# Performance work log

Hardware: AMD Instinct MI355X
Metric: run time of the kernel (lower is better)

Reference implementation:

```python
import jax, jax.numpy as jnp
import numpy as np
import math

DIM = 4096      # hidden size
NH = 32         # query heads
NKV = 8         # kv heads (GQA)
HD = 128        # head dim
SW = 4096       # sliding window / cache length
B = 8           # batch (decode)
START_POS = 2047
PAD_LEN = min(((START_POS + 1 + 31) // 32) * 32, SW)  # nearest_32 -> 2048
ROPE_THETA = 10000.0


def _rotation_matrix(pos, dhead, theta=ROPE_THETA):
    # freqs_to_rotation_matrix: block-diagonal 2x2 rotations, applied as q @ R
    freqs = 1.0 / (theta ** (np.arange(0, dhead, 2, dtype=np.float64) / dhead))
    ang = pos * freqs
    cos, sin = np.cos(ang), np.sin(ang)
    rot = np.zeros((dhead, dhead), dtype=np.float32)
    ev = np.arange(0, dhead, 2)
    od = ev + 1
    rot[ev, ev] = cos
    rot[od, od] = cos
    rot[ev, od] = -sin
    rot[od, ev] = sin
    return rot


def setup_inputs() -> dict:
    key = jax.random.key(0)
    ks = jax.random.split(key, 8)
    s = 0.02
    x = jax.random.normal(ks[0], (1, 1, B, DIM), jnp.float32)
    wq = jax.random.normal(ks[1], (DIM, NH * HD), jnp.float32) * s
    wk = jax.random.normal(ks[2], (DIM, NKV * HD), jnp.float32) * s
    wv = jax.random.normal(ks[3], (DIM, NKV * HD), jnp.float32) * s
    wo = jax.random.normal(ks[4], (NH * HD, DIM), jnp.float32) * s
    # true RoPE rotation matrix for the current position, same for all batch rows
    rot = jnp.asarray(_rotation_matrix(START_POS, HD))
    rot_mat = jnp.broadcast_to(rot, (1, B, HD, HD))
    # KV cache: valid history in [0, START_POS), rest is garbage that gets masked
    cache_k = jax.random.normal(ks[5], (B, NKV, SW, HD), jnp.float32) * s
    cache_v = jax.random.normal(ks[6], (B, NKV, SW, HD), jnp.float32) * s
    # additive mask: 0 for positions <= start_pos, finfo.min after
    neg = jnp.finfo(jnp.float32).min
    mask_row = jnp.where(jnp.arange(PAD_LEN) <= START_POS, 0.0, neg).astype(jnp.float32)
    attn_mask = jnp.broadcast_to(mask_row, (1, NH, B, PAD_LEN))
    return {
        "x": x, "wq": wq, "wk": wk, "wv": wv, "wo": wo,
        "rot_mat": rot_mat, "cache_k": cache_k, "cache_v": cache_v,
        "attn_mask": attn_mask, "start_pos": START_POS,
    }


def reference(x, wq, wk, wv, wo, rot_mat, cache_k, cache_v, attn_mask, start_pos):
    scale = 1.0 / math.sqrt(HD)
    xb = x[0, 0]                                  # (B, DIM)
    # fused QKV projection
    q = (xb @ wq).reshape(B, NH, HD)              # (B, NH, HD)
    k = (xb @ wk).reshape(B, NKV, HD)             # (B, NKV, HD)
    v = (xb @ wv).reshape(B, NKV, HD)             # (B, NKV, HD)
    # RoPE via explicit rotation-matrix matmul (per batch row)
    rm = rot_mat[0]                               # (B, HD, HD)
    q = jnp.einsum('bhd,bde->bhe', q, rm)
    k = jnp.einsum('bgd,bde->bge', k, rm)
    # update_cache at position `oldest` (= start_pos since start_pos < sliding_window)
    ck = cache_k.at[:, :, start_pos].set(k)
    cv = cache_v.at[:, :, start_pos].set(v)
    keys = ck[:, :, :PAD_LEN]                     # (B, NKV, L, HD)
    vals = cv[:, :, :PAD_LEN]                     # (B, NKV, L, HD)
    # grouped attention: NH query heads share NKV kv heads
    qg = q.reshape(B, NKV, NH // NKV, HD)
    scores = jnp.einsum('bgqd,bgld->bgql', qg, keys) * scale
    # attn_mask: (1, NH, B, L) -> (B, NKV, NH//NKV, L)
    mask = attn_mask[0].transpose(1, 0, 2).reshape(B, NKV, NH // NKV, PAD_LEN)
    probs = jax.nn.softmax(scores + mask, axis=-1)
    out = jnp.einsum('bgql,bgld->bgqd', probs, vals).reshape(B, NH * HD)
    dense = out @ wo                              # (B, DIM)
    return dense.reshape(1, 1, B, DIM)
```

## Files before the change

### kernel.cpp

```cpp
#include <hip/hip_runtime.h>
#include <math.h>

#define DIM 4096
#define NH 32
#define NKV 8
#define HD 128
#define B_ 8
#define SW 4096
#define PAD_LEN 2048
#define GQ 4
#define KSPLIT 16
#define KCHUNK 256
#define QKV_COLS (DIM + 2 * NKV * HD)
#define LCHUNK 256
#define NLCHUNK (PAD_LEN / LCHUNK)
#define SCALE 0.08838834764831845f

#define OFF_QKVP   0
#define OFF_Q      (OFF_QKVP + KSPLIT * B_ * QKV_COLS)
#define OFF_K      (OFF_Q + B_ * DIM)
#define OFF_V      (OFF_K + B_ * NKV * HD)
#define OFF_AP     (OFF_V + B_ * NKV * HD)
#define OFF_AO     (OFF_AP + B_ * NKV * NLCHUNK * GQ * (HD + 2))
#define OFF_OP     (OFF_AO + B_ * DIM)

__global__ void qkv_partial(const float* __restrict__ x,
                            const float* __restrict__ wq,
                            const float* __restrict__ wk,
                            const float* __restrict__ wv,
                            float* __restrict__ part) {
    __shared__ float xs[B_][KCHUNK];
    const int tid = threadIdx.x;
    const int col = blockIdx.x * 256 + tid;
    const int k0  = blockIdx.y * KCHUNK;

    #pragma unroll
    for (int i = 0; i < (B_ * KCHUNK) / 256; ++i) {
        int idx = i * 256 + tid;
        int r   = idx >> 8;
        int kk  = idx & (KCHUNK - 1);
        xs[r][kk] = x[r * DIM + k0 + kk];
    }
    __syncthreads();

    const float* W;
    int ldw, c;
    if (col < DIM)                { W = wq; ldw = NH * HD;  c = col; }
    else if (col < DIM + NKV*HD)  { W = wk; ldw = NKV * HD; c = col - DIM; }
    else                          { W = wv; ldw = NKV * HD; c = col - DIM - NKV * HD; }

    float acc[B_] = {0.f, 0.f, 0.f, 0.f, 0.f, 0.f, 0.f, 0.f};
    const float* wp = W + (size_t)k0 * ldw + c;
    #pragma unroll 4
    for (int kk = 0; kk < KCHUNK; ++kk) {
        float w = wp[(size_t)kk * ldw];
        #pragma unroll
        for (int r = 0; r < B_; ++r) acc[r] = fmaf(xs[r][kk], w, acc[r]);
    }
    #pragma unroll
    for (int r = 0; r < B_; ++r)
        part[((size_t)(blockIdx.y * B_ + r)) * QKV_COLS + col] = acc[r];
}

__global__ void qkv_reduce_rope(const float* __restrict__ part,
                                const float* __restrict__ rot,
                                float* __restrict__ qb,
                                float* __restrict__ kb,
                                float* __restrict__ vb) {
    const int tid = threadIdx.x;
    const int col = blockIdx.x * 256 + tid;
    const int r   = blockIdx.y;

    float v = 0.f;
    #pragma unroll
    for (int s = 0; s < KSPLIT; ++s)
        v += part[((size_t)(s * B_ + r)) * QKV_COLS + col];

    if (col < DIM + NKV * HD) {
        int hd = col & (HD - 1);
        int i2 = hd & ~1;
        const float* rm = rot + (size_t)r * HD * HD;
        float c = rm[i2 * HD + i2];
        float s = rm[(i2 + 1) * HD + i2];
        float partner = __shfl_xor(v, 1, 64);
        float outv = (hd & 1) ? (v * c - partner * s) : (v * c + partner * s);
        if (col < DIM) qb[r * DIM + col] = outv;
        else           kb[r * NKV * HD + (col - DIM)] = outv;
    } else {
        vb[r * NKV * HD + (col - DIM - NKV * HD)] = v;
    }
}

__global__ void attn_partial(const float* __restrict__ qb,
                             const float* __restrict__ knew,
                             const float* __restrict__ vnew,
                             const float* __restrict__ cache_k,
                             const float* __restrict__ cache_v,
                             const float* __restrict__ mask,
                             const int* __restrict__ start_pos_p,
                             float* __restrict__ part) {
    const int bg = blockIdx.x;
    const int b  = bg >> 3;
    const int g  = bg & 7;
    const int chunk = blockIdx.y;
    const int l0 = chunk * LCHUNK;
    const int tid = threadIdx.x;
    const int sp = start_pos_p[0];

    __shared__ float q_lds[GQ][HD];
    __shared__ float p_lds[GQ][LCHUNK];
    __shared__ float red[256];

    for (int i = tid; i < GQ * HD; i += 256) {
        int qh = i >> 7;
        int d  = i & (HD - 1);
        q_lds[qh][d] = qb[b * DIM + (g * GQ + qh) * HD + d];
    }
    __syncthreads();

    const int l = l0 + tid;
    const float* krow = (l == sp) ? (knew + (b * NKV + g) * HD)
                                  : (cache_k + (((size_t)(b * NKV + g)) * SW + l) * HD);
    float s[GQ] = {0.f, 0.f, 0.f, 0.f};
    const float4* k4 = (const float4*)krow;
    #pragma unroll 8
    for (int j = 0; j < HD / 4; ++j) {
        float4 kv = k4[j];
        #pragma unroll
        for (int qh = 0; qh < GQ; ++qh) {
            s[qh] += kv.x * q_lds[qh][4*j]   + kv.y * q_lds[qh][4*j+1]
                   + kv.z * q_lds[qh][4*j+2] + kv.w * q_lds[qh][4*j+3];
        }
    }

    float m[GQ], sum[GQ];
    for (int qh = 0; qh < GQ; ++qh) {
        float sv = s[qh] * SCALE
                 + mask[(((size_t)(g * GQ + qh)) * B_ + b) * PAD_LEN + l];
        red[tid] = sv; __syncthreads();
        for (int st = 128; st > 0; st >>= 1) {
            if (tid < st) red[tid] = fmaxf(red[tid], red[tid + st]);
            __syncthreads();
        }
        m[qh] = red[0]; __syncthreads();
        float p = __expf(sv - m[qh]);
        p_lds[qh][tid] = p;
        red[tid] = p; __syncthreads();
        for (int st = 128; st > 0; st >>= 1) {
            if (tid < st) red[tid] += red[tid + st];
            __syncthreads();
        }
        sum[qh] = red[0]; __syncthreads();
    }

    const int d  = tid & (HD - 1);
    const int h2 = tid >> 7;
    float acc0 = 0.f, acc1 = 0.f;
    for (int ll = 0; ll < LCHUNK; ++ll) {
        int lg = l0 + ll;
        float vv = (lg == sp) ? vnew[(b * NKV + g) * HD + d]
                              : cache_v[(((size_t)(b * NKV + g)) * SW + lg) * HD + d];
        acc0 = fmaf(p_lds[h2][ll],     vv, acc0);
        acc1 = fmaf(p_lds[h2 + 2][ll], vv, acc1);
    }

    const size_t base = ((size_t)bg * NLCHUNK + chunk) * GQ;
    part[(base + h2)     * (HD + 2) + 2 + d] = acc0;
    part[(base + h2 + 2) * (HD + 2) + 2 + d] = acc1;
    if (tid < GQ) {
        part[(base + tid) * (HD + 2) + 0] = m[tid];
        part[(base + tid) * (HD + 2) + 1] = sum[tid];
    }
}

__global__ void attn_combine(const float* __restrict__ part,
                             float* __restrict__ attnout) {
    const int bg = blockIdx.x;
    const int b  = bg >> 3;
    const int g  = bg & 7;
    const int d  = threadIdx.x;

    for (int qh = 0; qh < GQ; ++qh) {
        float M = -3.4e38f;
        #pragma unroll
        for (int c = 0; c < NLCHUNK; ++c)
            M = fmaxf(M, part[(((size_t)bg * NLCHUNK + c) * GQ + qh) * (HD + 2)]);
        float denom = 0.f, o = 0.f;
        #pragma unroll
        for (int c = 0; c < NLCHUNK; ++c) {
            const float* p = part + (((size_t)bg * NLCHUNK + c) * GQ + qh) * (HD + 2);
            float w = __expf(p[0] - M);
            denom += w * p[1];
            o     += w * p[2 + d];
        }
        attnout[b * DIM + (g * GQ + qh) * HD + d] = o / denom;
    }
}

__global__ void oproj_partial(const float* __restrict__ xin,
                              const float* __restrict__ wo,
                              float* __restrict__ part) {
    __shared__ float xs[B_][KCHUNK];
    const int tid = threadIdx.x;
    const int col = blockIdx.x * 256 + tid;
    const int k0  = blockIdx.y * KCHUNK;

    #pragma unroll
    for (int i = 0; i < (B_ * KCHUNK) / 256; ++i) {
        int idx = i * 256 + tid;
        int r   = idx >> 8;
        int kk  = idx & (KCHUNK - 1);
        xs[r][kk] = xin[r * DIM + k0 + kk];
    }
    __syncthreads();

    float acc[B_] = {0.f, 0.f, 0.f, 0.f, 0.f, 0.f, 0.f, 0.f};
    const float* wp = wo + (size_t)k0 * DIM + col;
    #pragma unroll 4
    for (int kk = 0; kk < KCHUNK; ++kk) {
        float w = wp[(size_t)kk * DIM];
        #pragma unroll
        for (int r = 0; r < B_; ++r) acc[r] = fmaf(xs[r][kk], w, acc[r]);
    }
    #pragma unroll
    for (int r = 0; r < B_; ++r)
        part[((size_t)(blockIdx.y * B_ + r)) * DIM + col] = acc[r];
}

__global__ void oproj_reduce(const float* __restrict__ part,
                             float* __restrict__ out) {
    const int tid = threadIdx.x;
    const int col = blockIdx.x * 256 + tid;
    const int r   = blockIdx.y;
    float v = 0.f;
    #pragma unroll
    for (int s = 0; s < KSPLIT; ++s)
        v += part[((size_t)(s * B_ + r)) * DIM + col];
    out[r * DIM + col] = v;
}

extern "C" void kernel_launch(void* const* d_in, const int* in_sizes, int n_in,
                              void* d_out, int out_size, void* d_ws, size_t ws_size,
                              hipStream_t stream) {
    const float* x        = (const float*)d_in[0];
    const float* wq       = (const float*)d_in[1];
    const float* wk       = (const float*)d_in[2];
    const float* wv       = (const float*)d_in[3];
    const float* wo       = (const float*)d_in[4];
    const float* rot      = (const float*)d_in[5];
    const float* cache_k  = (const float*)d_in[6];
    const float* cache_v  = (const float*)d_in[7];
    const float* mask     = (const float*)d_in[8];
    const int*   start_pp = (const int*)d_in[9];
    float* ws  = (float*)d_ws;
    float* out = (float*)d_out;

    dim3 gA(QKV_COLS / 256, KSPLIT);
    qkv_partial<<<gA, 256, 0, stream>>>(x, wq, wk, wv, ws + OFF_QKVP);

    dim3 gB(QKV_COLS / 256, B_);
    qkv_reduce_rope<<<gB, 256, 0, stream>>>(ws + OFF_QKVP, rot,
                                            ws + OFF_Q, ws + OFF_K, ws + OFF_V);

    dim3 gC(B_ * NKV, NLCHUNK);
    attn_partial<<<gC, 256, 0, stream>>>(ws + OFF_Q, ws + OFF_K, ws + OFF_V,
                                         cache_k, cache_v, mask, start_pp,
                                         ws + OFF_AP);

    attn_combine<<<dim3(B_ * NKV), 128, 0, stream>>>(ws + OFF_AP, ws + OFF_AO);

    dim3 gD(DIM / 256, KSPLIT);
    oproj_partial<<<gD, 256, 0, stream>>>(ws + OFF_AO, wo, ws + OFF_OP);

    dim3 gE(DIM / 256, B_);
    oproj_reduce<<<gE, 256, 0, stream>>>(ws + OFF_OP, out);
}
```

Before: 138.1 us.

## Widen split-K, vectorize GEMV loads, and use wave-shuffle softmax reductions

```diff
diff --git a/kernel.cpp b/kernel.cpp
--- a/kernel.cpp
+++ b/kernel.cpp
@@ -9,15 +9,17 @@
 #define SW 4096
 #define PAD_LEN 2048
 #define GQ 4
-#define KSPLIT 16
-#define KCHUNK 256
 #define QKV_COLS (DIM + 2 * NKV * HD)
+#define KSQ 64
+#define KCQ (DIM / KSQ)
+#define KSO 64
+#define KCO (DIM / KSO)
 #define LCHUNK 256
 #define NLCHUNK (PAD_LEN / LCHUNK)
 #define SCALE 0.08838834764831845f
 
 #define OFF_QKVP   0
-#define OFF_Q      (OFF_QKVP + KSPLIT * B_ * QKV_COLS)
+#define OFF_Q      (OFF_QKVP + KSQ * B_ * QKV_COLS)
 #define OFF_K      (OFF_Q + B_ * DIM)
 #define OFF_V      (OFF_K + B_ * NKV * HD)
 #define OFF_AP     (OFF_V + B_ * NKV * HD)
@@ -29,37 +31,47 @@
                             const float* __restrict__ wk,
                             const float* __restrict__ wv,
                             float* __restrict__ part) {
-    __shared__ float xs[B_][KCHUNK];
+    __shared__ float xs[B_][KCQ];
     const int tid = threadIdx.x;
-    const int col = blockIdx.x * 256 + tid;
-    const int k0  = blockIdx.y * KCHUNK;
-
-    #pragma unroll
-    for (int i = 0; i < (B_ * KCHUNK) / 256; ++i) {
-        int idx = i * 256 + tid;
-        int r   = idx >> 8;
-        int kk  = idx & (KCHUNK - 1);
-        xs[r][kk] = x[r * DIM + k0 + kk];
-    }
-    __syncthreads();
-
+    const int k0  = blockIdx.y * KCQ;
+
+    {
+        int idx = tid * 2;
+        int r   = idx >> 6;
+        int kk  = idx & (KCQ - 1);
+        float2 xv = *(const float2*)(x + r * DIM + k0 + kk);
+        xs[r][kk]     = xv.x;
+        xs[r][kk + 1] = xv.y;
+    }
+    __syncthreads();
+
+    const int bx = blockIdx.x;
     const float* W;
-    int ldw, c;
-    if (col < DIM)                { W = wq; ldw = NH * HD;  c = col; }
-    else if (col < DIM + NKV*HD)  { W = wk; ldw = NKV * HD; c = col - DIM; }
-    else                          { W = wv; ldw = NKV * HD; c = col - DIM - NKV * HD; }
-
-    float acc[B_] = {0.f, 0.f, 0.f, 0.f, 0.f, 0.f, 0.f, 0.f};
+    int ldw, cbase;
+    if (bx < 8)       { W = wq; ldw = NH * HD;  cbase = bx * 512; }
+    else if (bx < 10) { W = wk; ldw = NKV * HD; cbase = (bx - 8) * 512; }
+    else              { W = wv; ldw = NKV * HD; cbase = (bx - 10) * 512; }
+    const int c = cbase + tid * 2;
+
+    float2 acc[B_];
+    #pragma unroll
+    for (int r = 0; r < B_; ++r) { acc[r].x = 0.f; acc[r].y = 0.f; }
+
     const float* wp = W + (size_t)k0 * ldw + c;
-    #pragma unroll 4
-    for (int kk = 0; kk < KCHUNK; ++kk) {
-        float w = wp[(size_t)kk * ldw];
-        #pragma unroll
-        for (int r = 0; r < B_; ++r) acc[r] = fmaf(xs[r][kk], w, acc[r]);
-    }
+    #pragma unroll 8
+    for (int kk = 0; kk < KCQ; ++kk) {
+        float2 w = *(const float2*)(wp + (size_t)kk * ldw);
+        #pragma unroll
+        for (int r = 0; r < B_; ++r) {
+            float xv = xs[r][kk];
+            acc[r].x = fmaf(xv, w.x, acc[r].x);
+            acc[r].y = fmaf(xv, w.y, acc[r].y);
+        }
+    }
+    const int colg = bx * 512 + tid * 2;
     #pragma unroll
     for (int r = 0; r < B_; ++r)
-        part[((size_t)(blockIdx.y * B_ + r)) * QKV_COLS + col] = acc[r];
+        *(float2*)(part + ((size_t)(blockIdx.y * B_ + r)) * QKV_COLS + colg) = acc[r];
 }
 
 __global__ void qkv_reduce_rope(const float* __restrict__ part,
@@ -67,27 +79,30 @@
                                 float* __restrict__ qb,
                                 float* __restrict__ kb,
                                 float* __restrict__ vb) {
-    const int tid = threadIdx.x;
-    const int col = blockIdx.x * 256 + tid;
-    const int r   = blockIdx.y;
-
-    float v = 0.f;
-    #pragma unroll
-    for (int s = 0; s < KSPLIT; ++s)
-        v += part[((size_t)(s * B_ + r)) * QKV_COLS + col];
+    const int tid  = threadIdx.x;
+    const int col2 = blockIdx.x * 256 + tid;
+    const int col  = col2 * 2;
+    const int r    = blockIdx.y;
+
+    float2 v; v.x = 0.f; v.y = 0.f;
+    #pragma unroll 8
+    for (int s = 0; s < KSQ; ++s) {
+        float2 p = *(const float2*)(part + ((size_t)(s * B_ + r)) * QKV_COLS + col);
+        v.x += p.x; v.y += p.y;
+    }
 
     if (col < DIM + NKV * HD) {
         int hd = col & (HD - 1);
-        int i2 = hd & ~1;
         const float* rm = rot + (size_t)r * HD * HD;
-        float c = rm[i2 * HD + i2];
-        float s = rm[(i2 + 1) * HD + i2];
-        float partner = __shfl_xor(v, 1, 64);
-        float outv = (hd & 1) ? (v * c - partner * s) : (v * c + partner * s);
-        if (col < DIM) qb[r * DIM + col] = outv;
-        else           kb[r * NKV * HD + (col - DIM)] = outv;
+        float c  = rm[hd * HD + hd];
+        float sn = rm[(hd + 1) * HD + hd];
+        float2 o;
+        o.x = v.x * c + v.y * sn;
+        o.y = v.y * c - v.x * sn;
+        if (col < DIM) *(float2*)(qb + r * DIM + col) = o;
+        else           *(float2*)(kb + r * NKV * HD + (col - DIM)) = o;
     } else {
-        vb[r * NKV * HD + (col - DIM - NKV * HD)] = v;
+        *(float2*)(vb + r * NKV * HD + (col - DIM - NKV * HD)) = v;
     }
 }
 
@@ -109,7 +124,8 @@
 
     __shared__ float q_lds[GQ][HD];
     __shared__ float p_lds[GQ][LCHUNK];
-    __shared__ float red[256];
+    __shared__ float crossm[4][GQ];
+    __shared__ float crosss[4][GQ];
 
     for (int i = tid; i < GQ * HD; i += 256) {
         int qh = i >> 7;
@@ -132,41 +148,70 @@
                    + kv.z * q_lds[qh][4*j+2] + kv.w * q_lds[qh][4*j+3];
         }
     }
-
-    float m[GQ], sum[GQ];
+    float sv[GQ];
+    #pragma unroll
+    for (int qh = 0; qh < GQ; ++qh)
+        sv[qh] = s[qh] * SCALE
+               + mask[(((size_t)(g * GQ + qh)) * B_ + b) * PAD_LEN + l];
+
+    const int wave = tid >> 6;
+    const int lane = tid & 63;
+    float wm[GQ];
+    #pragma unroll
+    for (int qh = 0; qh < GQ; ++qh) wm[qh] = sv[qh];
+    #pragma unroll
+    for (int off = 32; off > 0; off >>= 1)
+        #pragma unroll
+        for (int qh = 0; qh < GQ; ++qh)
+            wm[qh] = fmaxf(wm[qh], __shfl_xor(wm[qh], off, 64));
+    if (lane == 0)
+        #pragma unroll
+        for (int qh = 0; qh < GQ; ++qh) crossm[wave][qh] = wm[qh];
+    __syncthreads();
+    float m[GQ];
+    #pragma unroll
+    for (int qh = 0; qh < GQ; ++qh)
+        m[qh] = fmaxf(fmaxf(crossm[0][qh], crossm[1][qh]),
+                      fmaxf(crossm[2][qh], crossm[3][qh]));
+
+    float wsum[GQ];
+    #pragma unroll
     for (int qh = 0; qh < GQ; ++qh) {
-        float sv = s[qh] * SCALE
-                 + mask[(((size_t)(g * GQ + qh)) * B_ + b) * PAD_LEN + l];
-        red[tid] = sv; __syncthreads();
-        for (int st = 128; st > 0; st >>= 1) {
-            if (tid < st) red[tid] = fmaxf(red[tid], red[tid + st]);
-            __syncthreads();
-        }
-        m[qh] = red[0]; __syncthreads();
-        float p = __expf(sv - m[qh]);
+        float p = __expf(sv[qh] - m[qh]);
         p_lds[qh][tid] = p;
-        red[tid] = p; __syncthreads();
-        for (int st = 128; st > 0; st >>= 1) {
-            if (tid < st) red[tid] += red[tid + st];
-            __syncthreads();
-        }
-        sum[qh] = red[0]; __syncthreads();
-    }
-
-    const int d  = tid & (HD - 1);
-    const int h2 = tid >> 7;
-    float acc0 = 0.f, acc1 = 0.f;
+        wsum[qh] = p;
+    }
+    #pragma unroll
+    for (int off = 32; off > 0; off >>= 1)
+        #pragma unroll
+        for (int qh = 0; qh < GQ; ++qh)
+            wsum[qh] += __shfl_xor(wsum[qh], off, 64);
+    if (lane == 0)
+        #pragma unroll
+        for (int qh = 0; qh < GQ; ++qh) crosss[wave][qh] = wsum[qh];
+    __syncthreads();
+    float sum[GQ];
+    #pragma unroll
+    for (int qh = 0; qh < GQ; ++qh)
+        sum[qh] = crosss[0][qh] + crosss[1][qh] + crosss[2][qh] + crosss[3][qh];
+
+    const int qh = wave;
+    const int d2 = lane * 2;
+    float2 acc; acc.x = 0.f; acc.y = 0.f;
+    const float* vbase = cache_v + (((size_t)(b * NKV + g)) * SW) * HD + d2;
+    const float* vnewp = vnew + (b * NKV + g) * HD + d2;
+    #pragma unroll 4
     for (int ll = 0; ll < LCHUNK; ++ll) {
         int lg = l0 + ll;
-        float vv = (lg == sp) ? vnew[(b * NKV + g) * HD + d]
-                              : cache_v[(((size_t)(b * NKV + g)) * SW + lg) * HD + d];
-        acc0 = fmaf(p_lds[h2][ll],     vv, acc0);
-        acc1 = fmaf(p_lds[h2 + 2][ll], vv, acc1);
+        const float* vp = (lg == sp) ? vnewp : (vbase + (size_t)lg * HD);
+        float2 vv = *(const float2*)vp;
+        float p = p_lds[qh][ll];
+        acc.x = fmaf(p, vv.x, acc.x);
+        acc.y = fmaf(p, vv.y, acc.y);
     }
 
     const size_t base = ((size_t)bg * NLCHUNK + chunk) * GQ;
-    part[(base + h2)     * (HD + 2) + 2 + d] = acc0;
-    part[(base + h2 + 2) * (HD + 2) + 2 + d] = acc1;
+    *(float2*)(part + (base + qh) * (HD + 2) + 2 + d2) = acc;
     if (tid < GQ) {
         part[(base + tid) * (HD + 2) + 0] = m[tid];
         part[(base + tid) * (HD + 2) + 1] = sum[tid];
@@ -200,43 +245,53 @@
 __global__ void oproj_partial(const float* __restrict__ xin,
                               const float* __restrict__ wo,
                               float* __restrict__ part) {
-    __shared__ float xs[B_][KCHUNK];
+    __shared__ float xs[B_][KCO];
     const int tid = threadIdx.x;
-    const int col = blockIdx.x * 256 + tid;
-    const int k0  = blockIdx.y * KCHUNK;
-
-    #pragma unroll
-    for (int i = 0; i < (B_ * KCHUNK) / 256; ++i) {
-        int idx = i * 256 + tid;
-        int r   = idx >> 8;
-        int kk  = idx & (KCHUNK - 1);
-        xs[r][kk] = xin[r * DIM + k0 + kk];
-    }
-    __syncthreads();
-
-    float acc[B_] = {0.f, 0.f, 0.f, 0.f, 0.f, 0.f, 0.f, 0.f};
+    const int k0  = blockIdx.y * KCO;
+
+    {
+        int idx = tid * 2;
+        int r   = idx >> 6;
+        int kk  = idx & (KCO - 1);
+        float2 xv = *(const float2*)(xin + r * DIM + k0 + kk);
+        xs[r][kk]     = xv.x;
+        xs[r][kk + 1] = xv.y;
+    }
+    __syncthreads();
+
+    const int col = blockIdx.x * 512 + tid * 2;
+    float2 acc[B_];
+    #pragma unroll
+    for (int r = 0; r < B_; ++r) { acc[r].x = 0.f; acc[r].y = 0.f; }
+
     const float* wp = wo + (size_t)k0 * DIM + col;
-    #pragma unroll 4
-    for (int kk = 0; kk < KCHUNK; ++kk) {
-        float w = wp[(size_t)kk * DIM];
-        #pragma unroll
-        for (int r = 0; r < B_; ++r) acc[r] = fmaf(xs[r][kk], w, acc[r]);
+    #pragma unroll 8
+    for (int kk = 0; kk < KCO; ++kk) {
+        float2 w = *(const float2*)(wp + (size_t)kk * DIM);
+        #pragma unroll
+        for (int r = 0; r < B_; ++r) {
+            float xv = xs[r][kk];
+            acc[r].x = fmaf(xv, w.x, acc[r].x);
+            acc[r].y = fmaf(xv, w.y, acc[r].y);
+        }
     }
     #pragma unroll
     for (int r = 0; r < B_; ++r)
-        part[((size_t)(blockIdx.y * B_ + r)) * DIM + col] = acc[r];
+        *(float2*)(part + ((size_t)(blockIdx.y * B_ + r)) * DIM + col) = acc[r];
 }
 
 __global__ void oproj_reduce(const float* __restrict__ part,
                              float* __restrict__ out) {
     const int tid = threadIdx.x;
-    const int col = blockIdx.x * 256 + tid;
+    const int col = (blockIdx.x * 256 + tid) * 2;
     const int r   = blockIdx.y;
-    float v = 0.f;
-    #pragma unroll
-    for (int s = 0; s < KSPLIT; ++s)
-        v += part[((size_t)(s * B_ + r)) * DIM + col];
-    out[r * DIM + col] = v;
+    float2 v; v.x = 0.f; v.y = 0.f;
+    #pragma unroll 8
+    for (int s = 0; s < KSO; ++s) {
+        float2 p = *(const float2*)(part + ((size_t)(s * B_ + r)) * DIM + col);
+        v.x += p.x; v.y += p.y;
+    }
+    *(float2*)(out + r * DIM + col) = v;
 }
 
 extern "C" void kernel_launch(void* const* d_in, const int* in_sizes, int n_in,
@@ -255,10 +310,10 @@
     float* ws  = (float*)d_ws;
     float* out = (float*)d_out;
 
-    dim3 gA(QKV_COLS / 256, KSPLIT);
+    dim3 gA(QKV_COLS / 512, KSQ);
     qkv_partial<<<gA, 256, 0, stream>>>(x, wq, wk, wv, ws + OFF_QKVP);
 
-    dim3 gB(QKV_COLS / 256, B_);
+    dim3 gB((QKV_COLS / 2) / 256, B_);
     qkv_reduce_rope<<<gB, 256, 0, stream>>>(ws + OFF_QKVP, rot,
                                             ws + OFF_Q, ws + OFF_K, ws + OFF_V);
 
@@ -269,9 +324,9 @@
 
     attn_combine<<<dim3(B_ * NKV), 128, 0, stream>>>(ws + OFF_AP, ws + OFF_AO);
 
-    dim3 gD(DIM / 256, KSPLIT);
+    dim3 gD(DIM / 512, KSO);
     oproj_partial<<<gD, 256, 0, stream>>>(ws + OFF_AO, wo, ws + OFF_OP);
 
-    dim3 gE(DIM / 256, B_);
+    dim3 gE((DIM / 2) / 256, B_);
     oproj_reduce<<<gE, 256, 0, stream>>>(ws + OFF_OP, out);
 }
```

After: 129.3 us. 1.07x faster.
